# Optimization experiments

Hardware: AMD Instinct MI355X
Metric: run time of the kernel (lower is better)

The kernel has to match this reference:

```python
import jax, jax.numpy as jnp
import numpy as np

DENSE_W = 0.7  # unused in learned fusion path but kept for parity
SPARSE_W = 0.3

def _l2norm(x):
    return x / jnp.linalg.norm(x, axis=-1, keepdims=True)

def setup_inputs() -> dict:
    key = jax.random.key(0)
    ks = jax.random.split(key, 8)
    Q, D, dim = 32, 4096, 384
    feat = 2 * dim + 2  # 770
    query_dense = _l2norm(jax.random.normal(ks[0], (Q, dim), jnp.float32))
    doc_dense = _l2norm(jax.random.normal(ks[1], (D, dim), jnp.float32))
    sparse_scores = jax.random.uniform(ks[2], (Q, D), jnp.float32)
    W1 = jax.random.normal(ks[3], (feat, 384), jnp.float32) * (1.0 / np.sqrt(feat))
    b1 = jnp.zeros((384,), jnp.float32)
    W2 = jax.random.normal(ks[4], (384, 192), jnp.float32) * (1.0 / np.sqrt(384))
    b2 = jnp.zeros((192,), jnp.float32)
    W3 = jax.random.normal(ks[5], (192, 1), jnp.float32) * (1.0 / np.sqrt(192))
    b3 = jnp.zeros((1,), jnp.float32)
    return {"query_dense": query_dense, "doc_dense": doc_dense,
            "sparse_scores": sparse_scores,
            "W1": W1, "b1": b1, "W2": W2, "b2": b2, "W3": W3, "b3": b3}

def reference(query_dense, doc_dense, sparse_scores, W1, b1, W2, b2, W3, b3):
    # dense cosine similarity (inputs are L2-normalized): [Q, D]
    dense_scores = query_dense @ doc_dense.T
    Q, D = dense_scores.shape
    dim = query_dense.shape[1]
    # Vectorized equivalent of the per-pair gather+concat double loop:
    # feature[q, d] = [query_dense[q], doc_dense[d], dense[q,d], sparse[q,d]]
    qf = jnp.broadcast_to(query_dense[:, None, :], (Q, D, dim))
    df = jnp.broadcast_to(doc_dense[None, :, :], (Q, D, dim))
    features = jnp.concatenate(
        [qf, df, dense_scores[..., None], sparse_scores[..., None]], axis=-1)  # [Q, D, 2*dim+2]
    # 4-layer fusion MLP (Dropout is identity at inference)
    h = jax.nn.relu(features @ W1 + b1)
    h = jax.nn.relu(h @ W2 + b2)
    fusion_weights = jax.nn.sigmoid((h @ W3 + b3)[..., 0])  # [Q, D]
    final_scores = fusion_weights * dense_scores + (1.0 - fusion_weights) * sparse_scores
    return final_scores, dense_scores, sparse_scores
```

## Files before the change

kernel.cpp:

```cpp
#include <hip/hip_runtime.h>
#include <hip/hip_bf16.h>

typedef __attribute__((ext_vector_type(2)))  float f32x2;
typedef __attribute__((ext_vector_type(4)))  float f32x4;
typedef __attribute__((ext_vector_type(16))) float f32x16;
typedef __attribute__((ext_vector_type(8)))  short bf16x8;
typedef __attribute__((ext_vector_type(2)))  unsigned int u32x2;
typedef __attribute__((ext_vector_type(4)))  unsigned int u32x4;

__device__ __forceinline__ short f2bf(float x){
    __hip_bfloat16 h = __float2bfloat16(x);
    return __builtin_bit_cast(short, h);
}
__device__ __forceinline__ float bf2f(short x){
    unsigned int u = ((unsigned int)(unsigned short)x) << 16;
    return __builtin_bit_cast(float, u);
}
__device__ __forceinline__ unsigned int cvt2(float lo, float hi){
    unsigned int r;
    asm("v_cvt_pk_bf16_f32 %0, %1, %2" : "=v"(r) : "v"(lo), "v"(hi));
    return r;
}

__global__ __launch_bounds__(256)
void pre0_kernel(const float* __restrict__ query, const float* __restrict__ doc,
                 const float* __restrict__ sparse, const float* __restrict__ W1,
                 const float* __restrict__ W2,
                 float* __restrict__ out_dense, float* __restrict__ out_sparse,
                 short* __restrict__ W1t, short* __restrict__ docb, short* __restrict__ qb16,
                 float* __restrict__ W1cdf, short* __restrict__ W2t){
    __shared__ float ldsq[32*388];
    __shared__ float ldsd[16*388];
    const int b = blockIdx.x, tid = threadIdx.x;

    if (b < 256){
        const int d0 = b*16;
        #pragma unroll
        for (int i=0;i<12;i++){ int idx = tid + i*256; int row = idx/96, c4 = idx%96;
            *(f32x4*)(ldsq + row*388 + c4*4) = *(const f32x4*)(query + row*384 + c4*4); }
        #pragma unroll
        for (int i=0;i<6;i++){ int idx = tid + i*256; int row = idx/96, c4 = idx%96;
            *(f32x4*)(ldsd + row*388 + c4*4) = *(const f32x4*)(doc + (d0+row)*384 + c4*4); }
        __syncthreads();
        const int q = tid>>3, dg = tid&7;
        const f32x4* q4  = (const f32x4*)(ldsq + q*388);
        const f32x4* d4a = (const f32x4*)(ldsd + dg*388);
        const f32x4* d4b = (const f32x4*)(ldsd + (dg+8)*388);
        f32x4 s0 = {0.f,0.f,0.f,0.f}, s1 = {0.f,0.f,0.f,0.f};
        #pragma unroll 4
        for (int k=0;k<96;k++){
            const f32x4 qv = q4[k];
            s0 += qv*d4a[k];
            s1 += qv*d4b[k];
        }
        out_dense[q*4096 + d0 + dg]     = s0[0]+s0[1]+s0[2]+s0[3];
        out_dense[q*4096 + d0 + dg + 8] = s1[0]+s1[1]+s1[2]+s1[3];
        if (tid < 128){
            int qq = tid>>2, c4 = tid&3;
            *(f32x4*)(out_sparse + qq*4096 + d0 + c4*4) = *(const f32x4*)(sparse + qq*4096 + d0 + c4*4);
        }
    } else if (b < 328){
        const int lt0 = (b-256)*256 + tid;
        #pragma unroll
        for (int i=0;i<2;i++){
            const int lt    = lt0 + i*18432;
            const int chunk = lt >> 6, lane = lt & 63;
            const int cl = lane & 15, quad = lane >> 4;
            const int half = (chunk >= 288) ? 1 : 0;
            const int cs = chunk - half*288;
            const int s = cs/24, ct = cs%24;
            const float* src = W1 + (half*384 + s*32 + quad*8)*384 + ct*16 + cl;
            float v[8];
            #pragma unroll
            for (int j=0;j<8;j++) v[j] = src[j*384];
            u32x4 o;
            o[0] = cvt2(v[0],v[1]); o[1] = cvt2(v[2],v[3]);
            o[2] = cvt2(v[4],v[5]); o[3] = cvt2(v[6],v[7]);
            *(u32x4*)(W1t + chunk*512 + lane*8) = o;
        }
    } else if (b < 424){
        const int t0 = (b-328)*256 + tid;
        #pragma unroll
        for (int i=0;i<16;i++){
            const int g = t0 + i*24576;
            const f32x4 v = *(const f32x4*)(doc + g*4);
            u32x2 o; o[0] = cvt2(v[0],v[1]); o[1] = cvt2(v[2],v[3]);
            *(u32x2*)(docb + g*4) = o;
        }
    } else if (b == 424){
        #pragma unroll
        for (int i=0;i<12;i++){
            const int g = tid + i*256;
            const f32x4 v = *(const f32x4*)(query + g*4);
            u32x2 o; o[0] = cvt2(v[0],v[1]); o[1] = cvt2(v[2],v[3]);
            *(u32x2*)(qb16 + g*4) = o;
        }
    } else if (b == 425){
        #pragma unroll
        for (int i=0;i<3;i++){
            int o = tid + i*256;
            W1cdf[o] = (o < 384) ? W1[768*384 + o] : W1[769*384 + (o - 384)];
        }
    } else {
        const int t0 = (b - 426)*256 + tid;
        #pragma unroll
        for (int i=0;i<9;i++){
            int c = t0 + i*1024;
            int lane_c = c & 63, st = c >> 6;
            int s = st/6, t2 = st%6;
            int n = t2*32 + (lane_c&31), kb = s*16 + ((lane_c>>5)&1)*8;
            bf16x8 v;
            #pragma unroll
            for (int j=0;j<8;j++) v[j] = f2bf(W2[(kb+j)*192 + n]);
            *(bf16x8*)(W2t + c*8) = v;
        }
    }
}

__global__ __launch_bounds__(256)
void pre1_kernel(const short* __restrict__ docb, const short* __restrict__ qb16,
                 const short* __restrict__ W1t, const float* __restrict__ b1,
                 short* __restrict__ Bws, float* __restrict__ Aq){
    const int b = blockIdx.x, tid = threadIdx.x;
    const int w = tid >> 6, lane = tid & 63;
    const int cl = lane & 15, quad = lane >> 4;

    const short* src; const short* wt; int r0; bool isA;
    if (b < 256){ r0 = b*16;       src = docb; wt = W1t + 147456; isA = false; }
    else        { r0 = (b-256)*16; src = qb16; wt = W1t;          isA = true;  }

    const short* ap = src + (r0+cl)*384 + quad*8;
    const short* wp = wt + (w*6)*512 + lane*8;

    f32x4 acc[6];
    #pragma unroll
    for (int t=0;t<6;t++) acc[t] = (f32x4){0.f,0.f,0.f,0.f};

    bf16x8 a_c = *(const bf16x8*)(ap);
    bf16x8 b_c[6];
    #pragma unroll
    for (int tt=0;tt<6;tt++) b_c[tt] = *(const bf16x8*)(wp + tt*512);

    #pragma unroll 1
    for (int s=0;s<12;s++){
        const int sn = (s < 11) ? s+1 : 0;
        const bf16x8 a_n = *(const bf16x8*)(ap + sn*32);
        bf16x8 b_n[6];
        #pragma unroll
        for (int tt=0;tt<6;tt++) b_n[tt] = *(const bf16x8*)(wp + sn*12288 + tt*512);
        #pragma unroll
        for (int tt=0;tt<6;tt++)
            acc[tt] = __builtin_amdgcn_mfma_f32_16x16x32_bf16(a_c, b_c[tt], acc[tt], 0, 0, 0);
        a_c = a_n;
        #pragma unroll
        for (int tt=0;tt<6;tt++) b_c[tt] = b_n[tt];
    }

    #pragma unroll
    for (int tt=0;tt<6;tt++){
        const int col = (w*6+tt)*16 + cl;
        if (isA){
            const float b1v = b1[col];
            #pragma unroll
            for (int r=0;r<4;r++)
                Aq[(r0 + quad*4 + r)*384 + col] = acc[tt][r] + b1v;
        } else {
            #pragma unroll
            for (int r=0;r<4;r++)
                Bws[(r0 + quad*4 + r)*384 + col] = f2bf(acc[tt][r]);
        }
    }
}

#define STEP(BW,A0,A1,S) do{                                                        \
    const int kf_ = (S)*16 + kbase;                                                 \
    const f32x4 wcA = *(const f32x4*)(lcd + kf_);                                   \
    const f32x4 wcB = *(const f32x4*)(lcd + kf_ + 4);                               \
    const f32x4 wdA = *(const f32x4*)(lcd + 384 + kf_);                             \
    const f32x4 wdB = *(const f32x4*)(lcd + 384 + kf_ + 4);                         \
    const short* lp_ = lw + ((S)*384 + lane)*8;                                     \
    const bf16x8 bfr0 = *(const bf16x8*)(lp_);                                      \
    const bf16x8 bfr1 = *(const bf16x8*)(lp_ + 512);                                \
    const bf16x8 bfr2 = *(const bf16x8*)(lp_ + 1024);                               \
    const bf16x8 bfr3 = *(const bf16x8*)(lp_ + 1536);                               \
    const bf16x8 bfr4 = *(const bf16x8*)(lp_ + 2048);                               \
    const bf16x8 bfr5 = *(const bf16x8*)(lp_ + 2560);                               \
    u32x4 frw_;                                                                     \
    { f32x2 h = {A0[0] + bf2f(BW[0]), A0[1] + bf2f(BW[1])};                         \
      h += dsv2 * (f32x2){wcA[0],wcA[1]}; h += ssv2 * (f32x2){wdA[0],wdA[1]};       \
      frw_[0] = cvt2(fmaxf(h[0],0.f), fmaxf(h[1],0.f)); }                           \
    { f32x2 h = {A0[2] + bf2f(BW[2]), A0[3] + bf2f(BW[3])};                         \
      h += dsv2 * (f32x2){wcA[2],wcA[3]}; h += ssv2 * (f32x2){wdA[2],wdA[3]};       \
      frw_[1] = cvt2(fmaxf(h[0],0.f), fmaxf(h[1],0.f)); }                           \
    { f32x2 h = {A1[0] + bf2f(BW[4]), A1[1] + bf2f(BW[5])};                         \
      h += dsv2 * (f32x2){wcB[0],wcB[1]}; h += ssv2 * (f32x2){wdB[0],wdB[1]};       \
      frw_[2] = cvt2(fmaxf(h[0],0.f), fmaxf(h[1],0.f)); }                           \
    { f32x2 h = {A1[2] + bf2f(BW[6]), A1[3] + bf2f(BW[7])};                         \
      h += dsv2 * (f32x2){wcB[2],wcB[3]}; h += ssv2 * (f32x2){wdB[2],wdB[3]};       \
      frw_[3] = cvt2(fmaxf(h[0],0.f), fmaxf(h[1],0.f)); }                           \
    const bf16x8 fr_ = __builtin_bit_cast(bf16x8, frw_);                            \
    acc[0] = __builtin_amdgcn_mfma_f32_32x32x16_bf16(fr_, bfr0, acc[0], 0, 0, 0);   \
    acc[1] = __builtin_amdgcn_mfma_f32_32x32x16_bf16(fr_, bfr1, acc[1], 0, 0, 0);   \
    acc[2] = __builtin_amdgcn_mfma_f32_32x32x16_bf16(fr_, bfr2, acc[2], 0, 0, 0);   \
    acc[3] = __builtin_amdgcn_mfma_f32_32x32x16_bf16(fr_, bfr3, acc[3], 0, 0, 0);   \
    acc[4] = __builtin_amdgcn_mfma_f32_32x32x16_bf16(fr_, bfr4, acc[4], 0, 0, 0);   \
    acc[5] = __builtin_amdgcn_mfma_f32_32x32x16_bf16(fr_, bfr5, acc[5], 0, 0, 0);   \
  }while(0)

__global__ __launch_bounds__(512, 2)
void main_kernel(const float* __restrict__ Aq, const short* __restrict__ Bws,
                 const float* __restrict__ W1cdf, const short* __restrict__ W2t,
                 const float* __restrict__ b2, const float* __restrict__ W3,
                 const float* __restrict__ b3, const float* __restrict__ sparse,
                 const float* __restrict__ dense_in, float* __restrict__ out_final){
    __shared__ __align__(16) short lw[73728];
    __shared__ __align__(16) float lcd[768];
    const int tid = threadIdx.x;

    #pragma unroll
    for (int i=0;i<18;i++){
        int c = tid + i*512;
        *(f32x4*)(lw + c*8) = *(const f32x4*)(W2t + c*8);
    }
    if (tid < 192)
        *(f32x4*)(lcd + tid*4) = *(const f32x4*)(W1cdf + tid*4);
    __syncthreads();

    const int lane = tid & 63, w = tid >> 6;
    const int m = lane & 31, q2 = lane >> 5;
    const int kbase = q2*8;
    const float b3v = b3[0];
    const int dcol0 = blockIdx.x*16 + w;

    const float dsv0 = dense_in[m*4096 + dcol0];
    const float ssv0 = sparse[m*4096 + dcol0];
    const float dsv1 = dense_in[m*4096 + dcol0 + 8];
    const float ssv1 = sparse[m*4096 + dcol0 + 8];

    #pragma unroll 1
    for (int t4=0; t4<2; t4++){
        const int dcol = dcol0 + t4*8;
        const float dsv = t4 ? dsv1 : dsv0;
        const float ssv = t4 ? ssv1 : ssv0;
        const f32x2 dsv2 = {dsv, dsv}, ssv2 = {ssv, ssv};

        f32x16 acc[6];
        #pragma unroll
        for (int t=0;t<6;t++)
            #pragma unroll
            for (int r=0;r<16;r++) acc[t][r] = 0.0f;

        const short* bp = Bws + dcol*384;
        const float* ap = Aq + m*384;

        bf16x8 bwA = *(const bf16x8*)(bp + kbase);
        f32x4  aA0 = *(const f32x4*)(ap + kbase);
        f32x4  aA1 = *(const f32x4*)(ap + kbase + 4);
        bf16x8 bwB = *(const bf16x8*)(bp + 16 + kbase);
        f32x4  aB0 = *(const f32x4*)(ap + 16 + kbase);
        f32x4  aB1 = *(const f32x4*)(ap + 16 + kbase + 4);
        bf16x8 bwC = *(const bf16x8*)(bp + 32 + kbase);
        f32x4  aC0 = *(const f32x4*)(ap + 32 + kbase);
        f32x4  aC1 = *(const f32x4*)(ap + 32 + kbase + 4);

        #pragma unroll 1
        for (int s=0; s<24; s+=3){
            STEP(bwA, aA0, aA1, s);
            { const int kp = (s+3 < 24) ? (s+3)*16 + kbase : kbase;
              bwA = *(const bf16x8*)(bp + kp);
              aA0 = *(const f32x4*)(ap + kp);
              aA1 = *(const f32x4*)(ap + kp + 4); }
            STEP(bwB, aB0, aB1, s+1);
            { const int kp = (s+4 < 24) ? (s+4)*16 + kbase : kbase;
              bwB = *(const bf16x8*)(bp + kp);
              aB0 = *(const f32x4*)(ap + kp);
              aB1 = *(const f32x4*)(ap + kp + 4); }
            STEP(bwC, aC0, aC1, s+2);
            { const int kp = (s+5 < 24) ? (s+5)*16 + kbase : kbase;
              bwC = *(const bf16x8*)(bp + kp);
              aC0 = *(const f32x4*)(ap + kp);
              aC1 = *(const f32x4*)(ap + kp + 4); }
        }

        float p[16];
        #pragma unroll
        for (int r=0;r<16;r++) p[r] = 0.0f;
        #pragma unroll
        for (int t=0;t<6;t++){
            const int n = t*32 + m;
            const float b2v = b2[n];
            const float w3v = W3[n];
            #pragma unroll
            for (int r=0;r<16;r++)
                p[r] += fmaxf(acc[t][r] + b2v, 0.0f) * w3v;
        }
        #pragma unroll
        for (int mask=1; mask<32; mask<<=1){
            #pragma unroll
            for (int r=0;r<16;r++) p[r] += __shfl_xor(p[r], mask);
        }
        float myp = p[0];
        #pragma unroll
        for (int r=1;r<16;r++) myp = (m==r) ? p[r] : myp;
        if (m < 16){
            const int row = (m&3) + 8*(m>>2) + 4*q2;
            float logit = myp + b3v;
            float wgt = 1.0f/(1.0f + __expf(-logit));
            float dd = dense_in[row*4096 + dcol];
            float ss = sparse[row*4096 + dcol];
            out_final[row*4096 + dcol] = wgt*dd + (1.0f - wgt)*ss;
        }
    }
}

extern "C" void kernel_launch(void* const* d_in, const int* in_sizes, int n_in,
                              void* d_out, int out_size, void* d_ws, size_t ws_size,
                              hipStream_t stream){
    const float* query  = (const float*)d_in[0];
    const float* doc    = (const float*)d_in[1];
    const float* sparse = (const float*)d_in[2];
    const float* W1     = (const float*)d_in[3];
    const float* b1     = (const float*)d_in[4];
    const float* W2     = (const float*)d_in[5];
    const float* b2     = (const float*)d_in[6];
    const float* W3     = (const float*)d_in[7];
    const float* b3     = (const float*)d_in[8];

    float* out_final  = (float*)d_out;
    float* out_dense  = (float*)d_out + 131072;
    float* out_sparse = (float*)d_out + 262144;

    short* Bws   = (short*)d_ws;
    float* Aq    = (float*)((char*)d_ws + 3145728);
    float* W1cdf = (float*)((char*)d_ws + 3194880);
    short* W2t   = (short*)((char*)d_ws + 3197952);
    short* W1t   = (short*)((char*)d_ws + 3345408);
    short* docb  = (short*)((char*)d_ws + 3935232);
    short* qb16  = (short*)((char*)d_ws + 7080960);

    hipLaunchKernelGGL(pre0_kernel, dim3(430), dim3(256), 0, stream,
                       query, doc, sparse, W1, W2, out_dense, out_sparse,
                       W1t, docb, qb16, W1cdf, W2t);
    hipLaunchKernelGGL(pre1_kernel, dim3(258), dim3(256), 0, stream,
                       docb, qb16, W1t, b1, Bws, Aq);
    hipLaunchKernelGGL(main_kernel, dim3(256), dim3(512), 0, stream,
                       Aq, Bws, W1cdf, W2t, b2, W3, b3, sparse, out_dense, out_final);
}
```

Measured before the change: 125.6 us.

## Switch main kernel to 16x16x32 MFMA with 1024-thread blocks

Replaces the 32x32x16 bf16 MFMA tiling in the main fused MLP kernel with 16x16x32 MFMAs. Two waves now split the 32 query rows of each doc column, and blocks grow to 1024 threads. The W2 pre-swizzle layout is rewritten to match the new B-fragment layout, and the row reduction shrinks to a 16-lane shuffle. The aim is fewer accumulator registers per wave and cheaper epilogue reductions, with more waves for latency hiding. The cost is a simpler single-stage prefetch and loss of the two-blocks-per-CU launch bound.

Measured after the change: 125.3 us. No clear change (-0.2%).

```diff
diff --git a/kernel.cpp b/kernel.cpp
--- a/kernel.cpp
+++ b/kernel.cpp
@@ -107,8 +107,8 @@
         for (int i=0;i<9;i++){
             int c = t0 + i*1024;
             int lane_c = c & 63, st = c >> 6;
-            int s = st/6, t2 = st%6;
-            int n = t2*32 + (lane_c&31), kb = s*16 + ((lane_c>>5)&1)*8;
+            int s = st/12, t2 = st%12;
+            int n = t2*16 + (lane_c&15), kb = s*32 + ((lane_c>>4)&3)*8;
             bf16x8 v;
             #pragma unroll
             for (int j=0;j<8;j++) v[j] = f2bf(W2[(kb+j)*192 + n]);
@@ -172,42 +172,7 @@
     }
 }
 
-#define STEP(BW,A0,A1,S) do{                                                        \
-    const int kf_ = (S)*16 + kbase;                                                 \
-    const f32x4 wcA = *(const f32x4*)(lcd + kf_);                                   \
-    const f32x4 wcB = *(const f32x4*)(lcd + kf_ + 4);                               \
-    const f32x4 wdA = *(const f32x4*)(lcd + 384 + kf_);                             \
-    const f32x4 wdB = *(const f32x4*)(lcd + 384 + kf_ + 4);                         \
-    const short* lp_ = lw + ((S)*384 + lane)*8;                                     \
-    const bf16x8 bfr0 = *(const bf16x8*)(lp_);                                      \
-    const bf16x8 bfr1 = *(const bf16x8*)(lp_ + 512);                                \
-    const bf16x8 bfr2 = *(const bf16x8*)(lp_ + 1024);                               \
-    const bf16x8 bfr3 = *(const bf16x8*)(lp_ + 1536);                               \
-    const bf16x8 bfr4 = *(const bf16x8*)(lp_ + 2048);                               \
-    const bf16x8 bfr5 = *(const bf16x8*)(lp_ + 2560);                               \
-    u32x4 frw_;                                                                     \
-    { f32x2 h = {A0[0] + bf2f(BW[0]), A0[1] + bf2f(BW[1])};                         \
-      h += dsv2 * (f32x2){wcA[0],wcA[1]}; h += ssv2 * (f32x2){wdA[0],wdA[1]};       \
-      frw_[0] = cvt2(fmaxf(h[0],0.f), fmaxf(h[1],0.f)); }                           \
-    { f32x2 h = {A0[2] + bf2f(BW[2]), A0[3] + bf2f(BW[3])};                         \
-      h += dsv2 * (f32x2){wcA[2],wcA[3]}; h += ssv2 * (f32x2){wdA[2],wdA[3]};       \
-      frw_[1] = cvt2(fmaxf(h[0],0.f), fmaxf(h[1],0.f)); }                           \
-    { f32x2 h = {A1[0] + bf2f(BW[4]), A1[1] + bf2f(BW[5])};                         \
-      h += dsv2 * (f32x2){wcB[0],wcB[1]}; h += ssv2 * (f32x2){wdB[0],wdB[1]};       \
-      frw_[2] = cvt2(fmaxf(h[0],0.f), fmaxf(h[1],0.f)); }                           \
-    { f32x2 h = {A1[2] + bf2f(BW[6]), A1[3] + bf2f(BW[7])};                         \
-      h += dsv2 * (f32x2){wcB[2],wcB[3]}; h += ssv2 * (f32x2){wdB[2],wdB[3]};       \
-      frw_[3] = cvt2(fmaxf(h[0],0.f), fmaxf(h[1],0.f)); }                           \
-    const bf16x8 fr_ = __builtin_bit_cast(bf16x8, frw_);                            \
-    acc[0] = __builtin_amdgcn_mfma_f32_32x32x16_bf16(fr_, bfr0, acc[0], 0, 0, 0);   \
-    acc[1] = __builtin_amdgcn_mfma_f32_32x32x16_bf16(fr_, bfr1, acc[1], 0, 0, 0);   \
-    acc[2] = __builtin_amdgcn_mfma_f32_32x32x16_bf16(fr_, bfr2, acc[2], 0, 0, 0);   \
-    acc[3] = __builtin_amdgcn_mfma_f32_32x32x16_bf16(fr_, bfr3, acc[3], 0, 0, 0);   \
-    acc[4] = __builtin_amdgcn_mfma_f32_32x32x16_bf16(fr_, bfr4, acc[4], 0, 0, 0);   \
-    acc[5] = __builtin_amdgcn_mfma_f32_32x32x16_bf16(fr_, bfr5, acc[5], 0, 0, 0);   \
-  }while(0)
-
-__global__ __launch_bounds__(512, 2)
+__global__ __launch_bounds__(1024)
 void main_kernel(const float* __restrict__ Aq, const short* __restrict__ Bws,
                  const float* __restrict__ W1cdf, const short* __restrict__ W2t,
                  const float* __restrict__ b2, const float* __restrict__ W3,
@@ -218,8 +183,8 @@
     const int tid = threadIdx.x;
 
     #pragma unroll
-    for (int i=0;i<18;i++){
-        int c = tid + i*512;
+    for (int i=0;i<9;i++){
+        int c = tid + i*1024;
         *(f32x4*)(lw + c*8) = *(const f32x4*)(W2t + c*8);
     }
     if (tid < 192)
@@ -227,87 +192,100 @@
     __syncthreads();
 
     const int lane = tid & 63, w = tid >> 6;
-    const int m = lane & 31, q2 = lane >> 5;
-    const int kbase = q2*8;
+    const int colslot = w >> 1, mhalf = w & 1;
+    const int cl = lane & 15, g = lane >> 4;
+    const int mrow = mhalf*16 + cl;
+    const int k8 = g*8;
     const float b3v = b3[0];
-    const int dcol0 = blockIdx.x*16 + w;
-
-    const float dsv0 = dense_in[m*4096 + dcol0];
-    const float ssv0 = sparse[m*4096 + dcol0];
-    const float dsv1 = dense_in[m*4096 + dcol0 + 8];
-    const float ssv1 = sparse[m*4096 + dcol0 + 8];
+    const int dcol0 = blockIdx.x*16 + colslot;
 
     #pragma unroll 1
     for (int t4=0; t4<2; t4++){
         const int dcol = dcol0 + t4*8;
-        const float dsv = t4 ? dsv1 : dsv0;
-        const float ssv = t4 ? ssv1 : ssv0;
+        const float dsv = dense_in[mrow*4096 + dcol];
+        const float ssv = sparse[mrow*4096 + dcol];
         const f32x2 dsv2 = {dsv, dsv}, ssv2 = {ssv, ssv};
 
-        f32x16 acc[6];
-        #pragma unroll
-        for (int t=0;t<6;t++)
-            #pragma unroll
-            for (int r=0;r<16;r++) acc[t][r] = 0.0f;
+        f32x4 acc[12];
+        #pragma unroll
+        for (int t=0;t<12;t++) acc[t] = (f32x4){0.f,0.f,0.f,0.f};
 
         const short* bp = Bws + dcol*384;
-        const float* ap = Aq + m*384;
-
-        bf16x8 bwA = *(const bf16x8*)(bp + kbase);
-        f32x4  aA0 = *(const f32x4*)(ap + kbase);
-        f32x4  aA1 = *(const f32x4*)(ap + kbase + 4);
-        bf16x8 bwB = *(const bf16x8*)(bp + 16 + kbase);
-        f32x4  aB0 = *(const f32x4*)(ap + 16 + kbase);
-        f32x4  aB1 = *(const f32x4*)(ap + 16 + kbase + 4);
-        bf16x8 bwC = *(const bf16x8*)(bp + 32 + kbase);
-        f32x4  aC0 = *(const f32x4*)(ap + 32 + kbase);
-        f32x4  aC1 = *(const f32x4*)(ap + 32 + kbase + 4);
+        const float* ap = Aq + mrow*384;
+
+        bf16x8 bwC = *(const bf16x8*)(bp + k8);
+        f32x4  aC0 = *(const f32x4*)(ap + k8);
+        f32x4  aC1 = *(const f32x4*)(ap + k8 + 4);
 
         #pragma unroll 1
-        for (int s=0; s<24; s+=3){
-            STEP(bwA, aA0, aA1, s);
-            { const int kp = (s+3 < 24) ? (s+3)*16 + kbase : kbase;
-              bwA = *(const bf16x8*)(bp + kp);
-              aA0 = *(const f32x4*)(ap + kp);
-              aA1 = *(const f32x4*)(ap + kp + 4); }
-            STEP(bwB, aB0, aB1, s+1);
-            { const int kp = (s+4 < 24) ? (s+4)*16 + kbase : kbase;
-              bwB = *(const bf16x8*)(bp + kp);
-              aB0 = *(const f32x4*)(ap + kp);
-              aB1 = *(const f32x4*)(ap + kp + 4); }
-            STEP(bwC, aC0, aC1, s+2);
-            { const int kp = (s+5 < 24) ? (s+5)*16 + kbase : kbase;
-              bwC = *(const bf16x8*)(bp + kp);
-              aC0 = *(const f32x4*)(ap + kp);
-              aC1 = *(const f32x4*)(ap + kp + 4); }
-        }
-
-        float p[16];
-        #pragma unroll
-        for (int r=0;r<16;r++) p[r] = 0.0f;
-        #pragma unroll
-        for (int t=0;t<6;t++){
-            const int n = t*32 + m;
+        for (int s=0; s<12; s++){
+            const int kn = (s < 11) ? (s+1)*32 + k8 : k8;
+            const bf16x8 bwN = *(const bf16x8*)(bp + kn);
+            const f32x4  aN0 = *(const f32x4*)(ap + kn);
+            const f32x4  aN1 = *(const f32x4*)(ap + kn + 4);
+
+            const int kf = s*32 + k8;
+            const f32x4 wcA = *(const f32x4*)(lcd + kf);
+            const f32x4 wcB = *(const f32x4*)(lcd + kf + 4);
+            const f32x4 wdA = *(const f32x4*)(lcd + 384 + kf);
+            const f32x4 wdB = *(const f32x4*)(lcd + 384 + kf + 4);
+
+            u32x4 frw;
+            { f32x2 h = {aC0[0] + bf2f(bwC[0]), aC0[1] + bf2f(bwC[1])};
+              h += dsv2 * (f32x2){wcA[0],wcA[1]}; h += ssv2 * (f32x2){wdA[0],wdA[1]};
+              frw[0] = cvt2(fmaxf(h[0],0.f), fmaxf(h[1],0.f)); }
+            { f32x2 h = {aC0[2] + bf2f(bwC[2]), aC0[3] + bf2f(bwC[3])};
+              h += dsv2 * (f32x2){wcA[2],wcA[3]}; h += ssv2 * (f32x2){wdA[2],wdA[3]};
+              frw[1] = cvt2(fmaxf(h[0],0.f), fmaxf(h[1],0.f)); }
+            { f32x2 h = {aC1[0] + bf2f(bwC[4]), aC1[1] + bf2f(bwC[5])};
+              h += dsv2 * (f32x2){wcB[0],wcB[1]}; h += ssv2 * (f32x2){wdB[0],wdB[1]};
+              frw[2] = cvt2(fmaxf(h[0],0.f), fmaxf(h[1],0.f)); }
+            { f32x2 h = {aC1[2] + bf2f(bwC[6]), aC1[3] + bf2f(bwC[7])};
+              h += dsv2 * (f32x2){wcB[2],wcB[3]}; h += ssv2 * (f32x2){wdB[2],wdB[3]};
+              frw[3] = cvt2(fmaxf(h[0],0.f), fmaxf(h[1],0.f)); }
+            const bf16x8 fr = __builtin_bit_cast(bf16x8, frw);
+
+            const short* lp = lw + s*6144 + lane*8;
+            #pragma unroll
+            for (int tg=0; tg<4; tg++){
+                const bf16x8 f0 = *(const bf16x8*)(lp + (tg*3+0)*512);
+                const bf16x8 f1 = *(const bf16x8*)(lp + (tg*3+1)*512);
+                const bf16x8 f2 = *(const bf16x8*)(lp + (tg*3+2)*512);
+                acc[tg*3+0] = __builtin_amdgcn_mfma_f32_16x16x32_bf16(fr, f0, acc[tg*3+0], 0, 0, 0);
+                acc[tg*3+1] = __builtin_amdgcn_mfma_f32_16x16x32_bf16(fr, f1, acc[tg*3+1], 0, 0, 0);
+                acc[tg*3+2] = __builtin_amdgcn_mfma_f32_16x16x32_bf16(fr, f2, acc[tg*3+2], 0, 0, 0);
+            }
+            bwC = bwN; aC0 = aN0; aC1 = aN1;
+        }
+
+        float p0=0.f, p1=0.f, p2=0.f, p3=0.f;
+        #pragma unroll
+        for (int t=0;t<12;t++){
+            const int n = t*16 + cl;
             const float b2v = b2[n];
             const float w3v = W3[n];
-            #pragma unroll
-            for (int r=0;r<16;r++)
-                p[r] += fmaxf(acc[t][r] + b2v, 0.0f) * w3v;
-        }
-        #pragma unroll
-        for (int mask=1; mask<32; mask<<=1){
-            #pragma unroll
-            for (int r=0;r<16;r++) p[r] += __shfl_xor(p[r], mask);
-        }
-        float myp = p[0];
-        #pragma unroll
-        for (int r=1;r<16;r++) myp = (m==r) ? p[r] : myp;
-        if (m < 16){
-            const int row = (m&3) + 8*(m>>2) + 4*q2;
-            float logit = myp + b3v;
-            float wgt = 1.0f/(1.0f + __expf(-logit));
-            float dd = dense_in[row*4096 + dcol];
-            float ss = sparse[row*4096 + dcol];
+            p0 += fmaxf(acc[t][0] + b2v, 0.0f) * w3v;
+            p1 += fmaxf(acc[t][1] + b2v, 0.0f) * w3v;
+            p2 += fmaxf(acc[t][2] + b2v, 0.0f) * w3v;
+            p3 += fmaxf(acc[t][3] + b2v, 0.0f) * w3v;
+        }
+        #pragma unroll
+        for (int mask=1; mask<16; mask<<=1){
+            p0 += __shfl_xor(p0, mask);
+            p1 += __shfl_xor(p1, mask);
+            p2 += __shfl_xor(p2, mask);
+            p3 += __shfl_xor(p3, mask);
+        }
+        float myp = p0;
+        myp = (cl==1) ? p1 : myp;
+        myp = (cl==2) ? p2 : myp;
+        myp = (cl==3) ? p3 : myp;
+        if (cl < 4){
+            const int row = mhalf*16 + g*4 + cl;
+            const float logit = myp + b3v;
+            const float wgt = 1.0f/(1.0f + __expf(-logit));
+            const float dd = dense_in[row*4096 + dcol];
+            const float ss = sparse[row*4096 + dcol];
             out_final[row*4096 + dcol] = wgt*dd + (1.0f - wgt)*ss;
         }
     }
@@ -343,6 +321,6 @@
                        W1t, docb, qb16, W1cdf, W2t);
     hipLaunchKernelGGL(pre1_kernel, dim3(258), dim3(256), 0, stream,
                        docb, qb16, W1t, b1, Bws, Aq);
-    hipLaunchKernelGGL(main_kernel, dim3(256), dim3(512), 0, stream,
+    hipLaunchKernelGGL(main_kernel, dim3(256), dim3(1024), 0, stream,
                        Aq, Bws, W1cdf, W2t, b2, W3, b3, sparse, out_dense, out_final);
 }
```
